# Kernel optimization log

Hardware: AMD Instinct MI355X
Metric: run time of the kernel (lower is better)

## Reference

```python
import jax, jax.numpy as jnp
import numpy as np

QMAX = 127.0  # int8 symmetric

def fake_quant(v):
    # symmetric per-tensor int8 quant -> dequant
    s = jnp.maximum(jnp.max(jnp.abs(v)), 1e-8) / QMAX
    return jnp.round(jnp.clip(v / s, -QMAX, QMAX)) * s

def setup_inputs() -> dict:
    key = jax.random.key(0)
    k1, k2, k3 = jax.random.split(key, 3)
    B, C, H, W = 64, 3, 224, 224
    D, P = 768, 8
    x = jax.random.normal(k1, (B, C, H, W), dtype=jnp.float32)
    w = jax.random.normal(k2, (D, C, P, P), dtype=jnp.float32) * 0.02
    b = jax.random.normal(k3, (D,), dtype=jnp.float32) * 0.02
    return {"x": x, "w": w, "b": b}

def reference(x, w, b):
    B, C, H, W = x.shape
    D, _, P, _ = w.shape
    gh, gw = H // P, W // P
    # quantized conv (HMQConv2d): fake-quant activations and weights, then patchify GEMM
    xq = fake_quant(x)
    wq = fake_quant(w)
    # extract non-overlapping PxP patches: [B, C, gh, P, gw, P]
    xp = xq.reshape(B, C, gh, P, gw, P)
    # conv stride=kernel=P  ==  patch matmul: out [B, gh, gw, D]
    out = jnp.einsum('bchpwq,dchq->bhwd', xp.transpose(0, 1, 2, 3, 4, 5), wq,
                     optimize=True) if False else jnp.einsum('bcxpyq,dcpq->bxyd', xp, wq)
    out = out + b
    # flatten(2).transpose(1,2): [B, N, D]
    out = out.reshape(B, gh * gw, D)
    # norm is Identity (norm_layer=None)
    return out
```

## Files before the change

### kernel.cpp

```cpp
#include <hip/hip_runtime.h>
#include <stdint.h>


typedef short bf16x8 __attribute__((ext_vector_type(8)));
using f32x4 = __attribute__((ext_vector_type(4))) float;

static __device__ __forceinline__ uint16_t f2bfbits(float f) {
  uint32_t u = __float_as_uint(f);
  u += 0x7FFFu + ((u >> 16) & 1u);
  return (uint16_t)(u >> 16);
}
static __device__ __forceinline__ uint32_t q2(float a, float b, float inv_s) {
  float qa = rintf(fminf(fmaxf(a * inv_s, -127.0f), 127.0f));
  float qb = rintf(fminf(fmaxf(b * inv_s, -127.0f), 127.0f));
  return (uint32_t)f2bfbits(qa) | ((uint32_t)f2bfbits(qb) << 16);
}
static __device__ __forceinline__ uint4 quant8(float4 a0, float4 a1, float inv_s) {
  uint4 q;
  q.x = q2(a0.x, a0.y, inv_s);
  q.y = q2(a0.z, a0.w, inv_s);
  q.z = q2(a1.x, a1.y, inv_s);
  q.w = q2(a1.z, a1.w, inv_s);
  return q;
}

#define NBX 1024
#define NBW 64
__global__ void absmax_k(const float4* __restrict__ x, int nx4,
                         const float4* __restrict__ w, int nw4,
                         float* __restrict__ partials) {
  __shared__ float red[4];
  float m = 0.0f;
  if (blockIdx.x < NBX) {
    for (int i = blockIdx.x * 256 + threadIdx.x; i < nx4; i += NBX * 256) {
      float4 u = x[i];
      m = fmaxf(m, fabsf(u.x)); m = fmaxf(m, fabsf(u.y));
      m = fmaxf(m, fabsf(u.z)); m = fmaxf(m, fabsf(u.w));
    }
  } else {
    for (int i = (blockIdx.x - NBX) * 256 + threadIdx.x; i < nw4; i += NBW * 256) {
      float4 u = w[i];
      m = fmaxf(m, fabsf(u.x)); m = fmaxf(m, fabsf(u.y));
      m = fmaxf(m, fabsf(u.z)); m = fmaxf(m, fabsf(u.w));
    }
  }
#pragma unroll
  for (int off = 32; off > 0; off >>= 1) m = fmaxf(m, __shfl_down(m, off, 64));
  if ((threadIdx.x & 63) == 0) red[threadIdx.x >> 6] = m;
  __syncthreads();
  if (threadIdx.x == 0) {
    m = fmaxf(fmaxf(red[0], red[1]), fmaxf(red[2], red[3]));
    partials[blockIdx.x] = m;
  }
}

__global__ void finalize_k(const float* __restrict__ partials,
                           float* __restrict__ slots) {
  __shared__ float red[16];
  int tid = threadIdx.x;
  float m = partials[tid];
#pragma unroll
  for (int off = 32; off > 0; off >>= 1) m = fmaxf(m, __shfl_down(m, off, 64));
  if ((tid & 63) == 0) red[tid >> 6] = m;
  __syncthreads();
  if (tid == 0) {
#pragma unroll
    for (int i = 1; i < 16; ++i) m = fmaxf(m, red[i]);
    slots[0] = fmaxf(m, 1e-8f) * (1.0f / 127.0f);
  }
  if (tid >= 64 && tid < 128) {
    float mw = partials[NBX + (tid - 64)];
#pragma unroll
    for (int off = 32; off > 0; off >>= 1) mw = fmaxf(mw, __shfl_down(mw, off, 64));
    if (tid == 64) slots[1] = fmaxf(mw, 1e-8f) * (1.0f / 127.0f);
  }
}

#define NQX 4704
#define NQW 72
__global__ void quant_xw_k(const float4* __restrict__ x,
                           const float4* __restrict__ w,
                           uint4* __restrict__ Aq, uint4* __restrict__ Wq,
                           const float* __restrict__ slots) {
  if (blockIdx.x < NQX) {
    int g = blockIdx.x * 256 + threadIdx.x;
    float inv = 1.0f / slots[0];
    float4 a0 = x[g * 2], a1 = x[g * 2 + 1];
    int gy = g % 28;
    int t  = g / 28;
    int h  = t % 224;
    int u2 = t / 224;
    int c  = u2 % 3;
    int b  = u2 / 3;
    int m  = b * 784 + (h >> 3) * 28 + gy;
    Aq[m * 24 + c * 8 + (h & 7)] = quant8(a0, a1, inv);
  } else {
    int g = (blockIdx.x - NQX) * 256 + threadIdx.x;
    float inv = 1.0f / slots[1];
    float4 a0 = w[g * 2], a1 = w[g * 2 + 1];
    Wq[g] = quant8(a0, a1, inv);
  }
}

__global__ __launch_bounds__(256) void gemm_k(
    const uint4* __restrict__ Aq, const uint4* __restrict__ Wq,
    const float* __restrict__ bias, const float* __restrict__ slots,
    float* __restrict__ out) {
  const int tid  = threadIdx.x;
  const int lane = tid & 63;
  const int wid  = tid >> 6;
  const int wm   = wid >> 1;
  const int wn   = wid & 1;
  const int lm   = lane & 15;
  const int lq   = lane >> 4;
  const int m0   = blockIdx.x * 128;
  const int n0   = blockIdx.y * 128;

  int abase[4], bbase[4];
#pragma unroll
  for (int tm = 0; tm < 4; ++tm)
    abase[tm] = (m0 + wm * 64 + tm * 16 + lm) * 24 + lq;
#pragma unroll
  for (int tn = 0; tn < 4; ++tn)
    bbase[tn] = (n0 + wn * 64 + tn * 16 + lm) * 24 + lq;

  f32x4 acc[4][4] = {};

#pragma unroll
  for (int ks = 0; ks < 6; ++ks) {
    bf16x8 af[4], bf[4];
#pragma unroll
    for (int tm = 0; tm < 4; ++tm)
      af[tm] = __builtin_bit_cast(bf16x8, Aq[abase[tm] + ks * 4]);
#pragma unroll
    for (int tn = 0; tn < 4; ++tn)
      bf[tn] = __builtin_bit_cast(bf16x8, Wq[bbase[tn] + ks * 4]);
#pragma unroll
    for (int tm = 0; tm < 4; ++tm)
#pragma unroll
      for (int tn = 0; tn < 4; ++tn)
        acc[tm][tn] = __builtin_amdgcn_mfma_f32_16x16x32_bf16(
            af[tm], bf[tn], acc[tm][tn], 0, 0, 0);
  }

  const float scale = slots[0] * slots[1];
#pragma unroll
  for (int tn = 0; tn < 4; ++tn) {
    int col = n0 + wn * 64 + tn * 16 + lm;
    float bv = bias[col];
#pragma unroll
    for (int tm = 0; tm < 4; ++tm) {
      int rbase = m0 + wm * 64 + tm * 16 + lq * 4;
#pragma unroll
      for (int r = 0; r < 4; ++r)
        out[(size_t)(rbase + r) * 768 + col] = acc[tm][tn][r] * scale + bv;
    }
  }
}


extern "C" void kernel_launch(void* const* d_in, const int* in_sizes, int n_in,
                              void* d_out, int out_size, void* d_ws, size_t ws_size,
                              hipStream_t stream) {
  const float4* x = (const float4*)d_in[0];
  const float4* w = (const float4*)d_in[1];
  const float* bias = (const float*)d_in[2];
  float* out = (float*)d_out;

  char* ws = (char*)d_ws;
  float* slots    = (float*)ws;
  float* partials = (float*)(ws + 256);
  uint4* Wq       = (uint4*)(ws + 8192);
  uint4* Aq       = (uint4*)(ws + 8192 + 294912);

  const int nx4 = 9633792 / 4;
  const int nw4 = 147456 / 4;

  absmax_k<<<NBX + NBW, 256, 0, stream>>>(x, nx4, w, nw4, partials);
  finalize_k<<<1, 1024, 0, stream>>>(partials, slots);
  quant_xw_k<<<NQX + NQW, 256, 0, stream>>>(x, w, Aq, Wq, slots);
  gemm_k<<<dim3(392, 6), 256, 0, stream>>>(Aq, Wq, bias, slots, out);
}
```

Before: 236.6 us.

## Fuse scale finalize into quant kernel, stage quant writes and GEMM epilogue through LDS

```diff
diff --git a/kernel.cpp b/kernel.cpp
--- a/kernel.cpp
+++ b/kernel.cpp
@@ -54,50 +54,57 @@
   }
 }
 
-__global__ void finalize_k(const float* __restrict__ partials,
-                           float* __restrict__ slots) {
-  __shared__ float red[16];
-  int tid = threadIdx.x;
-  float m = partials[tid];
-#pragma unroll
-  for (int off = 32; off > 0; off >>= 1) m = fmaxf(m, __shfl_down(m, off, 64));
-  if ((tid & 63) == 0) red[tid >> 6] = m;
+#define NQXB 1792
+#define NQWB 72
+__global__ __launch_bounds__(256) void quant_xw_k(
+    const float* __restrict__ x, const float4* __restrict__ w4,
+    uint4* __restrict__ Aq, uint4* __restrict__ Wq,
+    const float* __restrict__ partials, float* __restrict__ slots) {
+  __shared__ float redx[4];
+  __shared__ float redw_s;
+  __shared__ uint4 stg[28 * 25];
+  const int tid = threadIdx.x;
+
+  float mx = 0.0f;
+  for (int i = tid; i < NBX; i += 256) mx = fmaxf(mx, partials[i]);
+#pragma unroll
+  for (int off = 32; off > 0; off >>= 1) mx = fmaxf(mx, __shfl_down(mx, off, 64));
+  if ((tid & 63) == 0) redx[tid >> 6] = mx;
+  if (tid < 64) {
+    float mw = partials[NBX + tid];
+#pragma unroll
+    for (int off = 32; off > 0; off >>= 1) mw = fmaxf(mw, __shfl_down(mw, off, 64));
+    if (tid == 0) redw_s = mw;
+  }
   __syncthreads();
-  if (tid == 0) {
-#pragma unroll
-    for (int i = 1; i < 16; ++i) m = fmaxf(m, red[i]);
-    slots[0] = fmaxf(m, 1e-8f) * (1.0f / 127.0f);
-  }
-  if (tid >= 64 && tid < 128) {
-    float mw = partials[NBX + (tid - 64)];
-#pragma unroll
-    for (int off = 32; off > 0; off >>= 1) mw = fmaxf(mw, __shfl_down(mw, off, 64));
-    if (tid == 64) slots[1] = fmaxf(mw, 1e-8f) * (1.0f / 127.0f);
-  }
-}
-
-#define NQX 4704
-#define NQW 72
-__global__ void quant_xw_k(const float4* __restrict__ x,
-                           const float4* __restrict__ w,
-                           uint4* __restrict__ Aq, uint4* __restrict__ Wq,
-                           const float* __restrict__ slots) {
-  if (blockIdx.x < NQX) {
-    int g = blockIdx.x * 256 + threadIdx.x;
-    float inv = 1.0f / slots[0];
-    float4 a0 = x[g * 2], a1 = x[g * 2 + 1];
-    int gy = g % 28;
-    int t  = g / 28;
-    int h  = t % 224;
-    int u2 = t / 224;
-    int c  = u2 % 3;
-    int b  = u2 / 3;
-    int m  = b * 784 + (h >> 3) * 28 + gy;
-    Aq[m * 24 + c * 8 + (h & 7)] = quant8(a0, a1, inv);
+  float sx = fmaxf(fmaxf(redx[0], redx[1]), fmaxf(redx[2], redx[3]));
+  sx = fmaxf(sx, 1e-8f) * (1.0f / 127.0f);
+  float sw = fmaxf(redw_s, 1e-8f) * (1.0f / 127.0f);
+  if (blockIdx.x == 0 && tid == 0) { slots[0] = sx; slots[1] = sw; }
+
+  if (blockIdx.x < NQXB) {
+    const float inv = 1.0f / sx;
+    const int b  = blockIdx.x / 28;
+    const int gx = blockIdx.x - b * 28;
+    for (int t = tid; t < 672; t += 256) {
+      const int r  = t / 28;
+      const int gy = t - r * 28;
+      const int c = r >> 3, p = r & 7;
+      const float4* src =
+          (const float4*)(x + (size_t)((b * 3 + c) * 224 + gx * 8 + p) * 224);
+      float4 a0 = src[gy * 2], a1 = src[gy * 2 + 1];
+      stg[gy * 25 + r] = quant8(a0, a1, inv);
+    }
+    __syncthreads();
+    uint4* dst = Aq + (size_t)(b * 784 + gx * 28) * 24;
+    for (int t = tid; t < 672; t += 256) {
+      const int gy = t / 24;
+      dst[t] = stg[gy * 25 + (t - gy * 24)];
+    }
   } else {
-    int g = (blockIdx.x - NQX) * 256 + threadIdx.x;
-    float inv = 1.0f / slots[1];
-    float4 a0 = w[g * 2], a1 = w[g * 2 + 1];
+    const float inv = 1.0f / sw;
+    const int g = (blockIdx.x - NQXB) * 256 + tid;
+    float4 a0 = w4[g * 2], a1 = w4[g * 2 + 1];
     Wq[g] = quant8(a0, a1, inv);
   }
 }
@@ -106,6 +113,7 @@
     const uint4* __restrict__ Aq, const uint4* __restrict__ Wq,
     const float* __restrict__ bias, const float* __restrict__ slots,
     float* __restrict__ out) {
+  __shared__ float tr[4 * 1280];
   const int tid  = threadIdx.x;
   const int lane = tid & 63;
   const int wid  = tid >> 6;
@@ -144,17 +152,34 @@
   }
 
   const float scale = slots[0] * slots[1];
-#pragma unroll
-  for (int tn = 0; tn < 4; ++tn) {
-    int col = n0 + wn * 64 + tn * 16 + lm;
-    float bv = bias[col];
-#pragma unroll
-    for (int tm = 0; tm < 4; ++tm) {
-      int rbase = m0 + wm * 64 + tm * 16 + lq * 4;
-#pragma unroll
-      for (int r = 0; r < 4; ++r)
-        out[(size_t)(rbase + r) * 768 + col] = acc[tm][tn][r] * scale + bv;
-    }
+  float* T = &tr[wid * 1280];
+  const int c4 = lane & 15;
+  const int gc = n0 + wn * 64 + c4 * 4;
+  const float4 bv = *(const float4*)&bias[gc];
+
+#pragma unroll
+  for (int tm = 0; tm < 4; ++tm) {
+#pragma unroll
+    for (int tn = 0; tn < 4; ++tn)
+      *(f32x4*)&T[(tn * 16 + lm) * 20 + lq * 4] = acc[tm][tn];
+    asm volatile("s_waitcnt lgkmcnt(0)" ::: "memory");
+#pragma unroll
+    for (int i = 0; i < 4; ++i) {
+      const int s = (lane >> 4) + i * 4;
+      float4 v;
+      v.x = T[(c4 * 4 + 0) * 20 + s];
+      v.y = T[(c4 * 4 + 1) * 20 + s];
+      v.z = T[(c4 * 4 + 2) * 20 + s];
+      v.w = T[(c4 * 4 + 3) * 20 + s];
+      float4 o;
+      o.x = fmaf(v.x, scale, bv.x);
+      o.y = fmaf(v.y, scale, bv.y);
+      o.z = fmaf(v.z, scale, bv.z);
+      o.w = fmaf(v.w, scale, bv.w);
+      const int gm = m0 + wm * 64 + tm * 16 + s;
+      *(float4*)&out[(size_t)gm * 768 + gc] = o;
+    }
+    asm volatile("s_waitcnt lgkmcnt(0)" ::: "memory");
   }
 }
 
@@ -162,8 +187,9 @@
 extern "C" void kernel_launch(void* const* d_in, const int* in_sizes, int n_in,
                               void* d_out, int out_size, void* d_ws, size_t ws_size,
                               hipStream_t stream) {
-  const float4* x = (const float4*)d_in[0];
-  const float4* w = (const float4*)d_in[1];
+  const float* xf = (const float*)d_in[0];
+  const float4* x4 = (const float4*)d_in[0];
+  const float4* w4 = (const float4*)d_in[1];
   const float* bias = (const float*)d_in[2];
   float* out = (float*)d_out;
 
@@ -176,8 +202,7 @@
   const int nx4 = 9633792 / 4;
   const int nw4 = 147456 / 4;
 
-  absmax_k<<<NBX + NBW, 256, 0, stream>>>(x, nx4, w, nw4, partials);
-  finalize_k<<<1, 1024, 0, stream>>>(partials, slots);
-  quant_xw_k<<<NQX + NQW, 256, 0, stream>>>(x, w, Aq, Wq, slots);
+  absmax_k<<<NBX + NBW, 256, 0, stream>>>(x4, nx4, w4, nw4, partials);
+  quant_xw_k<<<NQXB + NQWB, 256, 0, stream>>>(xf, w4, Aq, Wq, partials, slots);
   gemm_k<<<dim3(392, 6), 256, 0, stream>>>(Aq, Wq, bias, slots, out);
 }
```

Result: no change. 232.7 us (-1.6%).
